# Kernel optimization log

Measured on AMD Instinct MI355X. Metric: run time of the kernel, lower is better.

The kernel has to match this reference:

```python
import jax, jax.numpy as jnp
import numpy as np

D_MODEL = 1024
NUM_HEADS = 16
D_K = D_MODEL // NUM_HEADS


def setup_inputs() -> dict:
    key = jax.random.key(0)
    ks = jax.random.split(key, 9)
    B, S = 4, 2048
    s = 1.0 / np.sqrt(D_MODEL)
    inp = {
        "x": jax.random.normal(ks[0], (B, S, D_MODEL), dtype=jnp.float32),
        "wq": jax.random.uniform(ks[1], (D_MODEL, D_MODEL), jnp.float32, -s, s),
        "bq": jax.random.uniform(ks[2], (D_MODEL,), jnp.float32, -s, s),
        "wk": jax.random.uniform(ks[3], (D_MODEL, D_MODEL), jnp.float32, -s, s),
        "bk": jax.random.uniform(ks[4], (D_MODEL,), jnp.float32, -s, s),
        "wv": jax.random.uniform(ks[5], (D_MODEL, D_MODEL), jnp.float32, -s, s),
        "bv": jax.random.uniform(ks[6], (D_MODEL,), jnp.float32, -s, s),
        "wo": jax.random.uniform(ks[7], (D_MODEL, D_MODEL), jnp.float32, -s, s),
        "bo": jax.random.uniform(ks[8], (D_MODEL,), jnp.float32, -s, s),
    }
    return inp


def reference(x, wq, bq, wk, bk, wv, bv, wo, bo):
    B, S, _ = x.shape
    H, Dk = NUM_HEADS, D_K
    # QKV projections; weights stored as (in, out) so y = x @ w + b
    q = (x @ wq + bq).reshape(B, S, H, Dk).transpose(0, 2, 1, 3)  # (B,H,S,Dk)
    k = (x @ wk + bk).reshape(B, S, H, Dk).transpose(0, 2, 1, 3)
    v = (x @ wv + bv).reshape(B, S, H, Dk).transpose(0, 2, 1, 3)
    scores = jnp.einsum("bhqd,bhkd->bhqk", q, k) / jnp.sqrt(jnp.float32(Dk))
    causal = jnp.tril(jnp.ones((S, S), dtype=bool))  # True = keep
    scores = jnp.where(causal, scores, jnp.float32(-jnp.inf))
    attn = jax.nn.softmax(scores, axis=-1)  # dropout=0 (eval)
    out = jnp.einsum("bhqk,bhkd->bhqd", attn, v)
    out = out.transpose(0, 2, 1, 3).reshape(B, S, H * Dk)
    return out @ wo + bo
```

## Files before the change

### kernel.cpp

```cpp
#include <hip/hip_runtime.h>
#include <hip/hip_bf16.h>


#define D_MODEL 1024
#define NHEADS  16
#define DK      64
#define BATCH   4
#define SEQ     2048
#define MROWS   (BATCH*SEQ)

typedef short bvec8 __attribute__((ext_vector_type(8)));
typedef float fvec4  __attribute__((ext_vector_type(4)));
typedef float fvec16 __attribute__((ext_vector_type(16)));

__device__ __forceinline__ unsigned short f2bf(float f) {
    unsigned int x = __float_as_uint(f);
    x += 0x7fffu + ((x >> 16) & 1u);
    return (unsigned short)(x >> 16);
}

__device__ __forceinline__ unsigned pack_bf16x2(float a, float b) {
#if __has_builtin(__builtin_amdgcn_cvt_pk_bf16_f32)
    typedef __bf16 bf16x2_t __attribute__((ext_vector_type(2)));
    union { bf16x2_t v; unsigned u; } cv;
    cv.v = __builtin_amdgcn_cvt_pk_bf16_f32(a, b);
    return cv.u;
#else
    return (unsigned)f2bf(a) | ((unsigned)f2bf(b) << 16);
#endif
}

__device__ __forceinline__ float fast_exp2(float x) {
#if __has_builtin(__builtin_amdgcn_exp2f)
    return __builtin_amdgcn_exp2f(x);
#else
    return exp2f(x);
#endif
}


__global__ void f32_to_bf16_k(const float* __restrict__ in,
                              unsigned short* __restrict__ out, int n4) {
    int i = blockIdx.x * 256 + threadIdx.x;
    if (i < n4) {
        float4 v = ((const float4*)in)[i];
        ushort4 o;
        o.x = f2bf(v.x); o.y = f2bf(v.y); o.z = f2bf(v.z); o.w = f2bf(v.w);
        ((ushort4*)out)[i] = o;
    }
}

__global__ void transpose_all_k(const float* __restrict__ wq, const float* __restrict__ wk,
                                const float* __restrict__ wv, const float* __restrict__ wo,
                                unsigned short* __restrict__ wqkvt,
                                unsigned short* __restrict__ wot) {
    __shared__ float tile[32][33];
    const int z = blockIdx.z;
    const float* W = (z == 0) ? wq : (z == 1) ? wk : (z == 2) ? wv : wo;
    unsigned short* Wt = (z == 3) ? wot : wqkvt + (size_t)z * D_MODEL * D_MODEL;
    int n0 = blockIdx.x * 32, k0 = blockIdx.y * 32;
    int tx = threadIdx.x & 31;
    int ty = (threadIdx.x >> 5) * 4;
#pragma unroll
    for (int i = 0; i < 4; ++i)
        tile[ty + i][tx] = W[(k0 + ty + i) * D_MODEL + n0 + tx];
    __syncthreads();
#pragma unroll
    for (int i = 0; i < 4; ++i)
        Wt[(n0 + ty + i) * D_MODEL + k0 + tx] = f2bf(tile[tx][ty + i]);
}

__global__ void build_cbias_k(const float* __restrict__ bq, const float* __restrict__ bk,
                              const float* __restrict__ bv, float* __restrict__ cb) {
    int i = blockIdx.x * 256 + threadIdx.x;
    float v = (i < 1024) ? bq[i] : (i < 2048) ? bk[i - 1024] : bv[i - 2048];
    cb[i] = v;
}

__global__ __launch_bounds__(256, 2)
void gemm_glds(const unsigned short* __restrict__ A,
               const unsigned short* __restrict__ Bt,
               const float* __restrict__ bias,
               unsigned short* __restrict__ oq,
               unsigned short* __restrict__ ok,
               unsigned short* __restrict__ ov,
               float* __restrict__ of,
               float qscale, int mode) {
    __shared__ __align__(16) unsigned short As[2][128 * 64];
    __shared__ __align__(16) unsigned short Bs[2][128 * 64];

    const int tid  = threadIdx.x;
    const int lane = tid & 63;
    const int w    = tid >> 6;
    const int wr   = w >> 1, wc = w & 1;
    const int quad = lane >> 4, l16 = lane & 15;
    const int rowBlock = blockIdx.y * 128;
    const int colBlock = blockIdx.x * 128;

    const int lrow   = lane >> 3;
    const int gchunk = (lane & 7) ^ lrow;

    fvec4 acc[4][4] = {};

    {
#pragma unroll
        for (int n = 0; n < 4; ++n) {
            const int g = w * 4 + n;
            __builtin_amdgcn_global_load_lds(
                (const __attribute__((address_space(1))) void*)
                    &A[(size_t)(rowBlock + g * 8 + lrow) * D_MODEL + gchunk * 8],
                (__attribute__((address_space(3))) void*)&As[0][g * 512], 16, 0, 0);
            __builtin_amdgcn_global_load_lds(
                (const __attribute__((address_space(1))) void*)
                    &Bt[(size_t)(colBlock + g * 8 + lrow) * D_MODEL + gchunk * 8],
                (__attribute__((address_space(3))) void*)&Bs[0][g * 512], 16, 0, 0);
        }
    }

    for (int i = 0; i < 16; ++i) {
        __syncthreads();
        const int buf = i & 1;
        if (i < 15) {
            const int k1 = (i + 1) * 64;
#pragma unroll
            for (int n = 0; n < 4; ++n) {
                const int g = w * 4 + n;
                __builtin_amdgcn_global_load_lds(
                    (const __attribute__((address_space(1))) void*)
                        &A[(size_t)(rowBlock + g * 8 + lrow) * D_MODEL + k1 + gchunk * 8],
                    (__attribute__((address_space(3))) void*)&As[buf ^ 1][g * 512], 16, 0, 0);
                __builtin_amdgcn_global_load_lds(
                    (const __attribute__((address_space(1))) void*)
                        &Bt[(size_t)(colBlock + g * 8 + lrow) * D_MODEL + k1 + gchunk * 8],
                    (__attribute__((address_space(3))) void*)&Bs[buf ^ 1][g * 512], 16, 0, 0);
            }
        }
#pragma unroll
        for (int kc = 0; kc < 2; ++kc) {
            bvec8 af[4], bfr[4];
#pragma unroll
            for (int ii = 0; ii < 4; ++ii) {
                int r = wr * 64 + ii * 16 + l16;
                af[ii] = *(const bvec8*)&As[buf][r * 64 + (((kc * 4 + quad) ^ (l16 & 7)) * 8)];
            }
#pragma unroll
            for (int j = 0; j < 4; ++j) {
                int r = wc * 64 + j * 16 + l16;
                bfr[j] = *(const bvec8*)&Bs[buf][r * 64 + (((kc * 4 + quad) ^ (l16 & 7)) * 8)];
            }
#pragma unroll
            for (int ii = 0; ii < 4; ++ii)
#pragma unroll
                for (int j = 0; j < 4; ++j)
                    acc[ii][j] = __builtin_amdgcn_mfma_f32_16x16x32_bf16(
                        af[ii], bfr[j], acc[ii][j], 0, 0, 0);
        }
    }

    if (mode == 0) {
#pragma unroll
        for (int i = 0; i < 4; ++i) {
#pragma unroll
            for (int j = 0; j < 4; ++j) {
                int ncol = colBlock + wc * 64 + j * 16 + l16;
                int which = ncol >> 10;
                int nn = ncol & 1023;
                int h = nn >> 6, d = nn & 63;
                float bv = bias[ncol];
#pragma unroll
                for (int r = 0; r < 4; ++r) {
                    int mrow = rowBlock + wr * 64 + i * 16 + quad * 4 + r;
                    int b = mrow >> 11, s = mrow & (SEQ - 1);
                    float v = acc[i][j][r] + bv;
                    if (which == 0)
                        oq[(((b * NHEADS + h) * SEQ + s) * DK) + d] = f2bf(v * qscale);
                    else if (which == 1)
                        ok[(((b * NHEADS + h) * SEQ + s) * DK) + d] = f2bf(v);
                    else
                        ov[(((b * NHEADS + h) * DK + d) * SEQ) + s] = f2bf(v);
                }
            }
        }
    } else {
#pragma unroll
        for (int i = 0; i < 4; ++i) {
#pragma unroll
            for (int j = 0; j < 4; ++j) {
                int ncol = colBlock + wc * 64 + j * 16 + l16;
                float bv = bias[ncol];
#pragma unroll
                for (int r = 0; r < 4; ++r) {
                    int mrow = rowBlock + wr * 64 + i * 16 + quad * 4 + r;
                    of[(size_t)mrow * D_MODEL + ncol] = acc[i][j][r] + bv;
                }
            }
        }
    }
}

__global__ __launch_bounds__(256, 4)
void attn_mfma9(const unsigned short* __restrict__ Q,
                const unsigned short* __restrict__ K,
                const unsigned short* __restrict__ Vt,
                unsigned short* __restrict__ O,
                float* __restrict__ Opart,
                float* __restrict__ Lpart) {
    __shared__ __align__(16) unsigned short Ksm[2][64 * 64];
    __shared__ __align__(16) unsigned short Vsm[2][64 * 64];
    __shared__ float Lsh[4][32];

    const int tid  = threadIdx.x;
    const int lane = tid & 63;
    const int wq   = tid >> 6;
    const int hf   = lane >> 5;
    const int l32  = lane & 31;
    const int hh = blockIdx.y, b = blockIdx.z;
    const int hb = b * NHEADS + hh;

    const int bx = blockIdx.x;
    int qt, kt0, kt1, slot;
    bool part;
    if (bx < 10) {
        qt   = 15 - (bx >> 1);
        const int half = bx & 1;
        slot = (qt - 11) * 2 + half;
        part = true;
        if (half == 0) { kt0 = 0;  kt1 = 17; }
        else           { kt0 = 17; kt1 = 2 * qt + 2; }
    } else {
        qt = 20 - bx; kt0 = 0; kt1 = 2 * qt + 2; part = false; slot = 0;
    }

    const size_t bhq = ((size_t)hb) * SEQ * DK;
    const unsigned short* Qb = Q + bhq;
    const unsigned short* Kb = K + bhq;
    const unsigned short* Vb = Vt + bhq;

    const int q0 = qt * 128 + wq * 32;

    bvec8 qf[4];
#pragma unroll
    for (int kc = 0; kc < 4; ++kc)
        qf[kc] = *(const bvec8*)&Qb[(q0 + l32) * DK + kc * 16 + hf * 8];

    const int sr = tid >> 2;
    const int sc = tid & 3;
    const int sp0 = ((sc) ^ (sr & 7)) * 8;
    const int sp1 = ((sc + 4) ^ (sr & 7)) * 8;

    const int ktact = 2 * qt + (wq >> 1);
    const int mofs  = (wq & 1) << 5;

    bvec8 kr0, kr1, vr0, vr1;
    {
        const unsigned short* kg = Kb + (kt0 * 64 + sr) * DK;
        kr0 = *(const bvec8*)(kg + sc * 8);
        kr1 = *(const bvec8*)(kg + (sc + 4) * 8);
        const unsigned short* vg = Vb + sr * SEQ + kt0 * 64;
        vr0 = *(const bvec8*)(vg + sc * 8);
        vr1 = *(const bvec8*)(vg + (sc + 4) * 8);
        *(bvec8*)&Ksm[0][sr * 64 + sp0] = kr0;
        *(bvec8*)&Ksm[0][sr * 64 + sp1] = kr1;
        *(bvec8*)&Vsm[0][sr * 64 + sp0] = vr0;
        *(bvec8*)&Vsm[0][sr * 64 + sp1] = vr1;
    }

    fvec16 acc0 = {};
    fvec16 acc1 = {};
    float lp = 0.f;

    for (int kt = kt0; kt < kt1; ++kt) {
        __syncthreads();
        const int buf = (kt - kt0) & 1;
        if (kt + 1 < kt1) {
            const unsigned short* kg = Kb + ((kt + 1) * 64 + sr) * DK;
            kr0 = *(const bvec8*)(kg + sc * 8);
            kr1 = *(const bvec8*)(kg + (sc + 4) * 8);
            const unsigned short* vg = Vb + sr * SEQ + (kt + 1) * 64;
            vr0 = *(const bvec8*)(vg + sc * 8);
            vr1 = *(const bvec8*)(vg + (sc + 4) * 8);
        }
        if (kt <= ktact) {
            const unsigned short* Kbuf = &Ksm[buf][0];
            const unsigned short* Vbuf = &Vsm[buf][0];

            fvec16 s0 = {}, s1 = {};
#pragma unroll
            for (int kc = 0; kc < 4; ++kc) {
                const int ch = (((kc * 2 + hf) ^ (l32 & 7)) * 8);
                bvec8 a0 = *(const bvec8*)&Kbuf[l32 * 64 + ch];
                bvec8 a1 = *(const bvec8*)&Kbuf[(32 + l32) * 64 + ch];
                s0 = __builtin_amdgcn_mfma_f32_32x32x16_bf16(a0, qf[kc], s0, 0, 0, 0);
                s1 = __builtin_amdgcn_mfma_f32_32x32x16_bf16(a1, qf[kc], s1, 0, 0, 0);
            }

            if (kt == ktact) {
#pragma unroll
                for (int r = 0; r < 16; ++r) {
                    const int key0 = (r & 3) + 8 * (r >> 2) + 4 * hf - mofs;
                    if (key0 > l32)      s0[r] = -__builtin_inff();
                    if (key0 + 32 > l32) s1[r] = -__builtin_inff();
                }
            }

            unsigned pk[16];
#pragma unroll
            for (int m = 0; m < 8; ++m) {
                float p0 = fast_exp2(s0[2 * m]);
                float p1 = fast_exp2(s0[2 * m + 1]);
                float p2 = fast_exp2(s1[2 * m]);
                float p3 = fast_exp2(s1[2 * m + 1]);
                lp += (p0 + p1) + (p2 + p3);
                pk[m]     = pack_bf16x2(p0, p1);
                pk[8 + m] = pack_bf16x2(p2, p3);
            }

#pragma unroll
            for (int kc16 = 0; kc16 < 4; ++kc16) {
                const int b0 = (kc16 >> 1) * 8 + (kc16 & 1) * 4;
                unsigned sw0 = __shfl_xor(pk[b0 + 0], 32);
                unsigned sw1 = __shfl_xor(pk[b0 + 1], 32);
                unsigned sw2 = __shfl_xor(pk[b0 + 2], 32);
                unsigned sw3 = __shfl_xor(pk[b0 + 3], 32);
                union { unsigned u[4]; bvec8 v; } afu;
                afu.u[0] = hf ? sw2 : pk[b0 + 0];
                afu.u[1] = hf ? sw3 : pk[b0 + 1];
                afu.u[2] = hf ? pk[b0 + 2] : sw0;
                afu.u[3] = hf ? pk[b0 + 3] : sw1;
                const int ch = (((kc16 * 2 + hf) ^ (l32 & 7)) * 8);
                bvec8 bv0 = *(const bvec8*)&Vbuf[l32 * 64 + ch];
                bvec8 bv1 = *(const bvec8*)&Vbuf[(32 + l32) * 64 + ch];
                acc0 = __builtin_amdgcn_mfma_f32_32x32x16_bf16(afu.v, bv0, acc0, 0, 0, 0);
                acc1 = __builtin_amdgcn_mfma_f32_32x32x16_bf16(afu.v, bv1, acc1, 0, 0, 0);
            }
        }
        if (kt + 1 < kt1) {
            const int nb = ((kt - kt0) & 1) ^ 1;
            *(bvec8*)&Ksm[nb][sr * 64 + sp0] = kr0;
            *(bvec8*)&Ksm[nb][sr * 64 + sp1] = kr1;
            *(bvec8*)&Vsm[nb][sr * 64 + sp0] = vr0;
            *(bvec8*)&Vsm[nb][sr * 64 + sp1] = vr1;
        }
    }

    const float l = lp + __shfl_xor(lp, 32);

    if (part) {
        if (lane < 32)
            Lpart[((size_t)slot * 64 + hb) * 128 + wq * 32 + l32] = l;
        float* Od = Opart + (((size_t)slot * 64 + hb) * 128 + wq * 32) * 64;
#pragma unroll
        for (int g = 0; g < 4; ++g)
#pragma unroll
            for (int rr = 0; rr < 4; ++rr) {
                const int reg = g * 4 + rr;
                const int qrl = g * 8 + 4 * hf + rr;
                Od[(size_t)qrl * 64 + l32]      = acc0[reg];
                Od[(size_t)qrl * 64 + 32 + l32] = acc1[reg];
            }
    } else {
        if (lane < 32) Lsh[wq][l32] = l;
#pragma unroll
        for (int g = 0; g < 4; ++g) {
            float4 lv = *(const float4*)&Lsh[wq][g * 8 + 4 * hf];
#pragma unroll
            for (int rr = 0; rr < 4; ++rr) {
                const int reg = g * 4 + rr;
                const int qrow = q0 + g * 8 + 4 * hf + rr;
                const float inv = 1.f / ((const float*)&lv)[rr];
                unsigned short* dst = O + (size_t)(b * SEQ + qrow) * D_MODEL + hh * DK + l32;
                dst[0]  = f2bf(acc0[reg] * inv);
                dst[32] = f2bf(acc1[reg] * inv);
            }
        }
    }
}

__global__ void attn_combine_k(const float* __restrict__ Opart,
                               const float* __restrict__ Lpart,
                               unsigned short* __restrict__ O) {
    const int qt = 11 + blockIdx.x;
    const int h = blockIdx.y, b = blockIdx.z;
    const int hb = b * NHEADS + h;
    const int s0 = (qt - 11) * 2;
    const float* A  = Opart + ((size_t)(s0)*64 + hb) * 128 * 64;
    const float* Bp = Opart + ((size_t)(s0 + 1) * 64 + hb) * 128 * 64;
    const float* LA = Lpart + ((size_t)(s0)*64 + hb) * 128;
    const float* LB = Lpart + ((size_t)(s0 + 1) * 64 + hb) * 128;
    for (int e = threadIdx.x; e < 128 * 64; e += 256) {
        const int qr = e >> 6, d = e & 63;
        const float inv = 1.f / (LA[qr] + LB[qr]);
        const float v = (A[e] + Bp[e]) * inv;
        O[(size_t)(b * SEQ + qt * 128 + qr) * D_MODEL + h * DK + d] = f2bf(v);
    }
}


extern "C" void kernel_launch(void* const* d_in, const int* in_sizes, int n_in,
                              void* d_out, int out_size, void* d_ws, size_t ws_size,
                              hipStream_t stream) {
    const float* x  = (const float*)d_in[0];
    const float* wq = (const float*)d_in[1];
    const float* bq = (const float*)d_in[2];
    const float* wk = (const float*)d_in[3];
    const float* bk = (const float*)d_in[4];
    const float* wv = (const float*)d_in[5];
    const float* bv = (const float*)d_in[6];
    const float* wo = (const float*)d_in[7];
    const float* bo = (const float*)d_in[8];
    float* out = (float*)d_out;

    char* ws = (char*)d_ws;
    const size_t MB = 1u << 20;
    unsigned short* xb    = (unsigned short*)(ws);
    unsigned short* wqkvt = (unsigned short*)(ws + 16 * MB);
    unsigned short* wot   = (unsigned short*)(ws + 22 * MB);
    unsigned short* qb    = (unsigned short*)(ws + 24 * MB);
    unsigned short* kb    = (unsigned short*)(ws + 40 * MB);
    unsigned short* vtb   = (unsigned short*)(ws + 56 * MB);
    unsigned short* ab    = (unsigned short*)(ws + 72 * MB);
    float* cbias = (float*)(ws + 72 * MB);
    float* Opart = (float*)(ws);
    float* Lpart = (float*)(ws + 21 * MB);

    f32_to_bf16_k<<<(MROWS * D_MODEL / 4 + 255) / 256, 256, 0, stream>>>(
        x, xb, MROWS * D_MODEL / 4);
    transpose_all_k<<<dim3(32, 32, 4), 256, 0, stream>>>(wq, wk, wv, wo, wqkvt, wot);
    build_cbias_k<<<12, 256, 0, stream>>>(bq, bk, bv, cbias);

    const float QSCALE = 0.125f * 1.44269504088896340736f;

    gemm_glds<<<dim3(3072 / 128, MROWS / 128), 256, 0, stream>>>(
        xb, wqkvt, cbias, qb, kb, vtb, nullptr, QSCALE, 0);

    attn_mfma9<<<dim3(21, NHEADS, BATCH), 256, 0, stream>>>(
        qb, kb, vtb, ab, Opart, Lpart);
    attn_combine_k<<<dim3(5, NHEADS, BATCH), 256, 0, stream>>>(Opart, Lpart, ab);

    gemm_glds<<<dim3(D_MODEL / 128, MROWS / 128), 256, 0, stream>>>(
        ab, wot, bo, nullptr, nullptr, nullptr, out, 1.0f, 1);
}
```

Baseline: 296.5 us.

## Split more causal query tiles into two halves and store partials as bf16

The causal attention work split now divides query tiles 8–15 into two key-range halves (split at the diagonal midpoint) instead of only tiles 11–15. A lookup table orders the 24 blocks per head so the heaviest pieces are scheduled first. Partial outputs are written as bf16 instead of fp32 to cut the partial-result traffic, and the combine kernel handles the 8 split tiles. This aims for better load balance across the grid, at the cost of more combine work and extra rounding of the unnormalized partial accumulators.

```diff
diff --git a/kernel.cpp b/kernel.cpp
--- a/kernel.cpp
+++ b/kernel.cpp
@@ -17,6 +17,9 @@
     unsigned int x = __float_as_uint(f);
     x += 0x7fffu + ((x >> 16) & 1u);
     return (unsigned short)(x >> 16);
+}
+__device__ __forceinline__ float bf2f(unsigned short u) {
+    return __uint_as_float(((unsigned int)u) << 16);
 }
 
 __device__ __forceinline__ unsigned pack_bf16x2(float a, float b) {
@@ -199,11 +202,11 @@
 }
 
 __global__ __launch_bounds__(256, 4)
-void attn_mfma9(const unsigned short* __restrict__ Q,
+void attn_mfmaA(const unsigned short* __restrict__ Q,
                 const unsigned short* __restrict__ K,
                 const unsigned short* __restrict__ Vt,
                 unsigned short* __restrict__ O,
-                float* __restrict__ Opart,
+                unsigned short* __restrict__ Opart,
                 float* __restrict__ Lpart) {
     __shared__ __align__(16) unsigned short Ksm[2][64 * 64];
     __shared__ __align__(16) unsigned short Vsm[2][64 * 64];
@@ -217,19 +220,17 @@
     const int hh = blockIdx.y, b = blockIdx.z;
     const int hb = b * NHEADS + hh;
 
+    static const int qt_tbl[24] = {15,15,7,14,14,6,13,13,12,12,5,11,
+                                   11,10,10,4,9,9,8,8,3,2,1,0};
+    static const int md_tbl[24] = {0,1,2,0,1,2,0,1,0,1,2,0,
+                                   1,0,1,2,0,1,0,1,2,2,2,2};
     const int bx = blockIdx.x;
-    int qt, kt0, kt1, slot;
-    bool part;
-    if (bx < 10) {
-        qt   = 15 - (bx >> 1);
-        const int half = bx & 1;
-        slot = (qt - 11) * 2 + half;
-        part = true;
-        if (half == 0) { kt0 = 0;  kt1 = 17; }
-        else           { kt0 = 17; kt1 = 2 * qt + 2; }
-    } else {
-        qt = 20 - bx; kt0 = 0; kt1 = 2 * qt + 2; part = false; slot = 0;
-    }
+    const int qt = qt_tbl[bx];
+    const int md = md_tbl[bx];
+    const bool part = (md < 2);
+    const int kt0 = (md == 1) ? qt + 1 : 0;
+    const int kt1 = (md == 0) ? qt + 1 : 2 * qt + 2;
+    const int slot = part ? ((qt - 8) * 2 + md) : 0;
 
     const size_t bhq = ((size_t)hb) * SEQ * DK;
     const unsigned short* Qb = Q + bhq;
@@ -348,15 +349,15 @@
     if (part) {
         if (lane < 32)
             Lpart[((size_t)slot * 64 + hb) * 128 + wq * 32 + l32] = l;
-        float* Od = Opart + (((size_t)slot * 64 + hb) * 128 + wq * 32) * 64;
+        unsigned short* Od = Opart + (((size_t)slot * 64 + hb) * 128 + wq * 32) * 64;
 #pragma unroll
         for (int g = 0; g < 4; ++g)
 #pragma unroll
             for (int rr = 0; rr < 4; ++rr) {
                 const int reg = g * 4 + rr;
                 const int qrl = g * 8 + 4 * hf + rr;
-                Od[(size_t)qrl * 64 + l32]      = acc0[reg];
-                Od[(size_t)qrl * 64 + 32 + l32] = acc1[reg];
+                Od[(size_t)qrl * 64 + l32]      = f2bf(acc0[reg]);
+                Od[(size_t)qrl * 64 + 32 + l32] = f2bf(acc1[reg]);
             }
     } else {
         if (lane < 32) Lsh[wq][l32] = l;
@@ -376,21 +377,21 @@
     }
 }
 
-__global__ void attn_combine_k(const float* __restrict__ Opart,
+__global__ void attn_combine_k(const unsigned short* __restrict__ Opart,
                                const float* __restrict__ Lpart,
                                unsigned short* __restrict__ O) {
-    const int qt = 11 + blockIdx.x;
+    const int qt = 8 + blockIdx.x;
     const int h = blockIdx.y, b = blockIdx.z;
     const int hb = b * NHEADS + h;
-    const int s0 = (qt - 11) * 2;
-    const float* A  = Opart + ((size_t)(s0)*64 + hb) * 128 * 64;
-    const float* Bp = Opart + ((size_t)(s0 + 1) * 64 + hb) * 128 * 64;
+    const int s0 = (qt - 8) * 2;
+    const unsigned short* A  = Opart + ((size_t)(s0)*64 + hb) * 128 * 64;
+    const unsigned short* Bp = Opart + ((size_t)(s0 + 1) * 64 + hb) * 128 * 64;
     const float* LA = Lpart + ((size_t)(s0)*64 + hb) * 128;
     const float* LB = Lpart + ((size_t)(s0 + 1) * 64 + hb) * 128;
     for (int e = threadIdx.x; e < 128 * 64; e += 256) {
         const int qr = e >> 6, d = e & 63;
         const float inv = 1.f / (LA[qr] + LB[qr]);
-        const float v = (A[e] + Bp[e]) * inv;
+        const float v = (bf2f(A[e]) + bf2f(Bp[e])) * inv;
         O[(size_t)(b * SEQ + qt * 128 + qr) * D_MODEL + h * DK + d] = f2bf(v);
     }
 }
@@ -420,8 +421,8 @@
     unsigned short* vtb   = (unsigned short*)(ws + 56 * MB);
     unsigned short* ab    = (unsigned short*)(ws + 72 * MB);
     float* cbias = (float*)(ws + 72 * MB);
-    float* Opart = (float*)(ws);
-    float* Lpart = (float*)(ws + 21 * MB);
+    unsigned short* Opart = (unsigned short*)(ws);
+    float* Lpart = (float*)(ws + 16 * MB);
 
     f32_to_bf16_k<<<(MROWS * D_MODEL / 4 + 255) / 256, 256, 0, stream>>>(
         x, xb, MROWS * D_MODEL / 4);
@@ -433,9 +434,9 @@
     gemm_glds<<<dim3(3072 / 128, MROWS / 128), 256, 0, stream>>>(
         xb, wqkvt, cbias, qb, kb, vtb, nullptr, QSCALE, 0);
 
-    attn_mfma9<<<dim3(21, NHEADS, BATCH), 256, 0, stream>>>(
+    attn_mfmaA<<<dim3(24, NHEADS, BATCH), 256, 0, stream>>>(
         qb, kb, vtb, ab, Opart, Lpart);
-    attn_combine_k<<<dim3(5, NHEADS, BATCH), 256, 0, stream>>>(Opart, Lpart, ab);
+    attn_combine_k<<<dim3(8, NHEADS, BATCH), 256, 0, stream>>>(Opart, Lpart, ab);
 
     gemm_glds<<<dim3(D_MODEL / 128, MROWS / 128), 256, 0, stream>>>(
         ab, wot, bo, nullptr, nullptr, nullptr, out, 1.0f, 1);
```

Result: no change. 296.4 us (-0.0%).
